# Kernel optimization log

Measured on AMD Instinct MI355X. Metric: run time of the kernel, lower is better.

Reference implementation:

```python
import jax, jax.numpy as jnp
import numpy as np

T, B, D, H = 512, 64, 512, 512

def setup_inputs() -> dict:
    key = jax.random.key(0)
    ks = jax.random.split(key, 12)
    s_in = 1.0 / np.sqrt(D + H)
    s_res = 1.0 / np.sqrt(D)
    inp = {
        'inputs': jax.random.normal(ks[0], (T, B, D), jnp.float32),
        'W_f': jax.random.uniform(ks[1], (H, D + H), jnp.float32, -s_in, s_in),
        'b_f': jax.random.uniform(ks[2], (H,), jnp.float32, -s_in, s_in),
        'W_i': jax.random.uniform(ks[3], (H, D + H), jnp.float32, -s_in, s_in),
        'b_i': jax.random.uniform(ks[4], (H,), jnp.float32, -s_in, s_in),
        'W_g': jax.random.uniform(ks[5], (H, D + H), jnp.float32, -s_in, s_in),
        'b_g': jax.random.uniform(ks[6], (H,), jnp.float32, -s_in, s_in),
        'W_o': jax.random.uniform(ks[7], (H, D + H), jnp.float32, -s_in, s_in),
        'b_o': jax.random.uniform(ks[8], (H,), jnp.float32, -s_in, s_in),
        'W_r': jax.random.uniform(ks[9], (H, D), jnp.float32, -s_res, s_res),
        'b_r': jax.random.uniform(ks[10], (H,), jnp.float32, -s_res, s_res),
    }
    return inp

def reference(inputs, W_f, b_f, W_i, b_i, W_g, b_g, W_o, b_o, W_r, b_r):
    Bsz = inputs.shape[1]
    Hd = W_f.shape[0]
    # residual projection is independent of recurrence: batch it over all timesteps
    res = jnp.einsum('tbd,hd->tbh', inputs, W_r) + b_r  # [T,B,H]

    def step(carry, xr):
        hx, cx = carry
        x, r = xr
        combined = jnp.concatenate([x, hx], axis=1)  # [B, D+H]
        f = jax.nn.sigmoid(combined @ W_f.T + b_f)
        i = jax.nn.sigmoid(combined @ W_i.T + b_i)
        g = jnp.tanh(combined @ W_g.T + b_g)
        o = jax.nn.sigmoid(combined @ W_o.T + b_o)
        cx = f * cx + i * g
        hx = o * jnp.tanh(cx) + r  # use_residual=True
        return (hx, cx), hx

    hx0 = jnp.zeros((Bsz, Hd), inputs.dtype)
    cx0 = jnp.zeros((Bsz, Hd), inputs.dtype)
    (hx, cx), stacked = jax.lax.scan(step, (hx0, cx0), (inputs, res))
    return stacked, (hx, cx)
```

## Files before the change

### kernel.cpp

```cpp
#include <hip/hip_runtime.h>


typedef __bf16         bfrag8 __attribute__((ext_vector_type(8)));
typedef float          f32x4v __attribute__((ext_vector_type(4)));
typedef unsigned short u16x8  __attribute__((ext_vector_type(8)));
typedef int            v4i    __attribute__((ext_vector_type(4)));

#define N_TB    32768
#define GXW     2560
#define OUT_HX  16777216
#define OUT_CX  16809984

__device__ __forceinline__ float bf2f(unsigned short u) {
  unsigned int x = ((unsigned int)u) << 16;
  return __builtin_bit_cast(float, x);
}
__device__ __forceinline__ unsigned short f2bf(float f) {
  unsigned int x = __builtin_bit_cast(unsigned int, f);
  x = x + 0x7FFFu + ((x >> 16) & 1u);
  return (unsigned short)(x >> 16);
}
__device__ __forceinline__ float sigf(float x) {
  x = fminf(fmaxf(x, -30.f), 30.f);
  return 1.f / (1.f + __expf(-x));
}
__device__ __forceinline__ float tanh_f(float x) {
  x = fminf(fmaxf(x, -15.f), 15.f);
  float e = __expf(-2.f * x);
  return (1.f - e) / (1.f + e);
}

__global__ void cvt_kernel(const float* __restrict__ in, unsigned short* __restrict__ out) {
  int i = (blockIdx.x * 256 + threadIdx.x) * 4;
  float4 v = *(const float4*)(in + i);
  ushort4 o = make_ushort4(f2bf(v.x), f2bf(v.y), f2bf(v.z), f2bf(v.w));
  *(ushort4*)(out + i) = o;
}

__global__ void repack_kernel(const float* __restrict__ Wf, const float* __restrict__ Wi,
                              const float* __restrict__ Wg, const float* __restrict__ Wo,
                              const float* __restrict__ Wr,
                              const float* __restrict__ bfp, const float* __restrict__ bip,
                              const float* __restrict__ bgp, const float* __restrict__ bop,
                              const float* __restrict__ brp,
                              unsigned short* __restrict__ Wc, unsigned short* __restrict__ Whx,
                              float* __restrict__ bias) {
  int tid = blockIdx.x * 256 + threadIdx.x;
  if (tid < 262144) {
    int row = tid >> 7;
    int k4  = (tid & 127) * 4;
    int g = row >> 9, h = row & 511;
    const float* W = (g == 0) ? Wf : (g == 1) ? Wi : (g == 2) ? Wg : Wo;
    float4 a = *(const float4*)(W + (size_t)h * 1024 + k4);
    float4 b = *(const float4*)(W + (size_t)h * 1024 + 512 + k4);
    *(ushort4*)(Wc  + (size_t)row * 512 + k4) = make_ushort4(f2bf(a.x), f2bf(a.y), f2bf(a.z), f2bf(a.w));
    *(ushort4*)(Whx + (size_t)row * 512 + k4) = make_ushort4(f2bf(b.x), f2bf(b.y), f2bf(b.z), f2bf(b.w));
  } else if (tid < 327680) {
    int t2 = tid - 262144;
    int row = t2 >> 7;
    int k4  = (t2 & 127) * 4;
    float4 a = *(const float4*)(Wr + (size_t)row * 512 + k4);
    *(ushort4*)(Wc + (size_t)(2048 + row) * 512 + k4) =
        make_ushort4(f2bf(a.x), f2bf(a.y), f2bf(a.z), f2bf(a.w));
  }
  if (tid < 2560) {
    float v;
    if      (tid <  512) v = bfp[tid];
    else if (tid < 1024) v = bip[tid - 512];
    else if (tid < 1536) v = bgp[tid - 1024];
    else if (tid < 2048) v = bop[tid - 1536];
    else                 v = brp[tid - 2048];
    bias[tid] = v;
  }
}

__global__ __launch_bounds__(256)
void gemm_kernel(const unsigned short* __restrict__ A, const unsigned short* __restrict__ B,
                 const float* __restrict__ bias, unsigned short* __restrict__ C) {
  const int bm = blockIdx.x;
  const int bn = blockIdx.y;
  const int tid = threadIdx.x;
  const int lane = tid & 63;
  const int w = tid >> 6;
  const int wm = w & 1, wn = w >> 1;
  const int col = lane & 15, q = lane >> 4;

  __shared__ unsigned short As[128 * 64] __attribute__((aligned(16)));
  __shared__ unsigned short Bs[128 * 64] __attribute__((aligned(16)));

  f32x4v acc[4][4] = {};

  for (int kt = 0; kt < 8; ++kt) {
    __syncthreads();
    #pragma unroll
    for (int p = 0; p < 4; ++p) {
      int idx = p * 256 + tid;
      int row = idx >> 3, gc = idx & 7;
      *(u16x8*)(&As[idx * 8]) = *(const u16x8*)(A + (size_t)(bm * 128 + row) * 512 + kt * 64 + gc * 8);
      *(u16x8*)(&Bs[idx * 8]) = *(const u16x8*)(B + (size_t)(bn * 128 + row) * 512 + kt * 64 + gc * 8);
    }
    __syncthreads();
    #pragma unroll
    for (int kk = 0; kk < 2; ++kk) {
      bfrag8 af[4], bfr[4];
      #pragma unroll
      for (int mt = 0; mt < 4; ++mt)
        af[mt] = *(const bfrag8*)(&As[(wm * 64 + mt * 16 + col) * 64 + kk * 32 + q * 8]);
      #pragma unroll
      for (int nt = 0; nt < 4; ++nt)
        bfr[nt] = *(const bfrag8*)(&Bs[(wn * 64 + nt * 16 + col) * 64 + kk * 32 + q * 8]);
      #pragma unroll
      for (int mt = 0; mt < 4; ++mt)
        #pragma unroll
        for (int nt = 0; nt < 4; ++nt)
          acc[mt][nt] = __builtin_amdgcn_mfma_f32_16x16x32_bf16(af[mt], bfr[nt], acc[mt][nt], 0, 0, 0);
    }
  }
  #pragma unroll
  for (int mt = 0; mt < 4; ++mt) {
    const int m0 = bm * 128 + wm * 64 + mt * 16 + q * 4;
    const float4 b4 = *(const float4*)(bias + m0);
    #pragma unroll
    for (int nt = 0; nt < 4; ++nt) {
      const int n = bn * 128 + wn * 64 + nt * 16 + col;
      f32x4v v = acc[mt][nt];
      ushort4 o = make_ushort4(f2bf(v[0] + b4.x), f2bf(v[1] + b4.y),
                               f2bf(v[2] + b4.z), f2bf(v[3] + b4.w));
      *(ushort4*)(C + (size_t)n * GXW + m0) = o;
    }
  }
}

__global__ __launch_bounds__(256, 1)
void recur_kernel(const unsigned short* __restrict__ Whx, const unsigned short* __restrict__ gx,
                  unsigned short* __restrict__ hbuf, int* flags, float* __restrict__ out) {
  const int jb = blockIdx.x;
  const int tid = threadIdx.x;
  const int lane = tid & 63;
  const int w = tid >> 6;
  const int gp = w & 1;
  const int mh = w >> 1;
  const int col = lane & 15;
  const int q = lane >> 4;

  __shared__ float S[2][4][64][20] __attribute__((aligned(16)));
  __shared__ unsigned short Hs[64][520] __attribute__((aligned(16)));

  bfrag8 Bf[4][8];
  #pragma unroll
  for (int g = 0; g < 4; ++g) {
    const unsigned short* wp = Whx + (size_t)(g * 512 + jb * 16 + col) * 512 + gp * 256 + q * 8;
    #pragma unroll
    for (int kk = 0; kk < 8; ++kk)
      Bf[g][kk] = *(const bfrag8*)(wp + kk * 32);
  }

  const int ub = tid >> 2;
  const int ucg = (tid & 3) * 4;
  float c4[4] = {0.f, 0.f, 0.f, 0.f};

  ushort4 gxv[4], rv;
  {
    const unsigned short* g0 = gx + (size_t)ub * GXW + jb * 16 + ucg;
    #pragma unroll
    for (int gg = 0; gg < 4; ++gg) gxv[gg] = *(const ushort4*)(g0 + gg * 512);
    rv = *(const ushort4*)(g0 + 2048);
  }

  for (int t = 0; t < 512; ++t) {
    if (t > 0) {
      if (tid < 32) {
        while (__hip_atomic_load(flags + tid, __ATOMIC_RELAXED, __HIP_MEMORY_SCOPE_AGENT) < t) {
        }
      }
      __syncthreads();
    }

    {
      const char* hsrc = (const char*)(hbuf + (t & 1) * 32768);
      v4i tmp[16];
      #pragma unroll
      for (int i = 0; i < 16; ++i) {
        const char* p = hsrc + (size_t)(i * 256 + tid) * 16;
        asm volatile("global_load_dwordx4 %0, %1, off sc0 sc1"
                     : "=v"(tmp[i]) : "v"(p) : "memory");
      }
      asm volatile("s_waitcnt vmcnt(0)" ::: "memory");
      #pragma unroll
      for (int i = 0; i < 16; ++i) {
        int idx = i * 256 + tid;
        *(v4i*)((char*)&Hs[0][0] + (size_t)(idx >> 6) * 1040 + (idx & 63) * 16) = tmp[i];
      }
    }
    __syncthreads();

    bfrag8 Af[2][8];
    #pragma unroll
    for (int mt = 0; mt < 2; ++mt) {
      const unsigned short* ap = &Hs[mh * 32 + mt * 16 + col][gp * 256 + q * 8];
      #pragma unroll
      for (int kk = 0; kk < 8; ++kk)
        Af[mt][kk] = *(const bfrag8*)(ap + kk * 32);
    }
    f32x4v acc[2][4] = {};
    #pragma unroll
    for (int kk = 0; kk < 8; ++kk)
      #pragma unroll
      for (int mt = 0; mt < 2; ++mt)
        #pragma unroll
        for (int g = 0; g < 4; ++g)
          acc[mt][g] = __builtin_amdgcn_mfma_f32_16x16x32_bf16(Af[mt][kk], Bf[g][kk], acc[mt][g], 0, 0, 0);

    #pragma unroll
    for (int mt = 0; mt < 2; ++mt)
      #pragma unroll
      for (int g = 0; g < 4; ++g) {
        const int b0 = mh * 32 + mt * 16 + q * 4;
        #pragma unroll
        for (int r = 0; r < 4; ++r)
          S[gp][g][b0 + r][col] = acc[mt][g][r];
      }
    __syncthreads();

    float pre[4][4];
    #pragma unroll
    for (int gg = 0; gg < 4; ++gg) {
      float4 s0 = *(const float4*)&S[0][gg][ub][ucg];
      float4 s1 = *(const float4*)&S[1][gg][ub][ucg];
      pre[gg][0] = s0.x + s1.x + bf2f(gxv[gg].x);
      pre[gg][1] = s0.y + s1.y + bf2f(gxv[gg].y);
      pre[gg][2] = s0.z + s1.z + bf2f(gxv[gg].z);
      pre[gg][3] = s0.w + s1.w + bf2f(gxv[gg].w);
    }
    float rres[4] = {bf2f(rv.x), bf2f(rv.y), bf2f(rv.z), bf2f(rv.w)};
    float hv[4];
    #pragma unroll
    for (int j = 0; j < 4; ++j) {
      float fg = sigf(pre[0][j]);
      float ig = sigf(pre[1][j]);
      float gg = tanh_f(pre[2][j]);
      float og = sigf(pre[3][j]);
      c4[j] = fg * c4[j] + ig * gg;
      hv[j] = og * tanh_f(c4[j]) + rres[j];
    }
    float4 h4 = make_float4(hv[0], hv[1], hv[2], hv[3]);

    if (t < 511) {
      ushort4 hb4 = make_ushort4(f2bf(hv[0]), f2bf(hv[1]), f2bf(hv[2]), f2bf(hv[3]));
      union { ushort4 u4; unsigned long long u64; } pk;
      pk.u4 = hb4;
      __hip_atomic_store((unsigned long long*)(hbuf + ((t + 1) & 1) * 32768 + ub * 512 + jb * 16 + ucg),
                         pk.u64, __ATOMIC_RELAXED, __HIP_MEMORY_SCOPE_AGENT);
      asm volatile("s_waitcnt vmcnt(0)" ::: "memory");
      __syncthreads();
      if (tid == 0)
        __hip_atomic_store(flags + jb, t + 1, __ATOMIC_RELAXED, __HIP_MEMORY_SCOPE_AGENT);
    }

    *(float4*)(out + (size_t)t * 32768 + ub * 512 + jb * 16 + ucg) = h4;

    if (t == 511) {
      *(float4*)(out + OUT_HX + ub * 512 + jb * 16 + ucg) = h4;
      *(float4*)(out + OUT_CX + ub * 512 + jb * 16 + ucg) = make_float4(c4[0], c4[1], c4[2], c4[3]);
    } else {
      const unsigned short* gn = gx + (size_t)((t + 1) * 64 + ub) * GXW + jb * 16 + ucg;
      #pragma unroll
      for (int gg = 0; gg < 4; ++gg) gxv[gg] = *(const ushort4*)(gn + gg * 512);
      rv = *(const ushort4*)(gn + 2048);
    }
  }
}

extern "C" void kernel_launch(void* const* d_in, const int* in_sizes, int n_in,
                              void* d_out, int out_size, void* d_ws, size_t ws_size,
                              hipStream_t stream) {
  const float* inputs = (const float*)d_in[0];
  const float* Wf = (const float*)d_in[1];
  const float* bf_ = (const float*)d_in[2];
  const float* Wi = (const float*)d_in[3];
  const float* bi_ = (const float*)d_in[4];
  const float* Wg = (const float*)d_in[5];
  const float* bg_ = (const float*)d_in[6];
  const float* Wo = (const float*)d_in[7];
  const float* bo_ = (const float*)d_in[8];
  const float* Wr = (const float*)d_in[9];
  const float* br_ = (const float*)d_in[10];
  float* out = (float*)d_out;

  unsigned short* X    = (unsigned short*)d_ws;
  unsigned short* Wc   = X + 16777216;
  unsigned short* Whx  = Wc + 1310720;
  float*          bias = (float*)(Whx + 1048576);
  unsigned short* gx   = (unsigned short*)(bias + 2560);
  unsigned short* hbuf = gx + 83886080;
  int*            flags = (int*)(hbuf + 65536);
  const size_t ws_needed = 206186624;
  if (ws_size < ws_needed) return;

  hipMemsetAsync(hbuf, 0, 65536 * 2 + 32 * 4, stream);

  cvt_kernel<<<16384, 256, 0, stream>>>(inputs, X);
  repack_kernel<<<1280, 256, 0, stream>>>(Wf, Wi, Wg, Wo, Wr, bf_, bi_, bg_, bo_, br_,
                                          Wc, Whx, bias);
  gemm_kernel<<<dim3(20, 256), 256, 0, stream>>>(Wc, X, bias, gx);
  recur_kernel<<<32, 256, 0, stream>>>(Whx, gx, hbuf, flags, out);
}
```

Baseline: 2.498 ms.

## Load recurrent h fragments directly from global and split gates across 8 waves

The recurrent kernel now runs 512 threads per block, with each wave owning two gates instead of four, which halves the weight fragments held per wave and the MFMAs each wave issues per step. The LDS staging of h is dropped: each wave loads its MFMA A-fragments straight from the global h buffer, which removes one LDS round trip and one block barrier per timestep. The next step's gx and residual loads are issued early, before the MFMAs, so their latency overlaps with compute. The cost is redundant global loads of h, since waves sharing rows each fetch the same data, and more threads that must meet at the remaining barriers.

```diff
diff --git a/kernel.cpp b/kernel.cpp
--- a/kernel.cpp
+++ b/kernel.cpp
@@ -131,41 +131,45 @@
   }
 }
 
-__global__ __launch_bounds__(256, 1)
+__global__ __launch_bounds__(512, 1)
 void recur_kernel(const unsigned short* __restrict__ Whx, const unsigned short* __restrict__ gx,
                   unsigned short* __restrict__ hbuf, int* flags, float* __restrict__ out) {
   const int jb = blockIdx.x;
   const int tid = threadIdx.x;
   const int lane = tid & 63;
   const int w = tid >> 6;
-  const int gp = w & 1;
-  const int mh = w >> 1;
+  const int gh = w & 1;
+  const int gp = (w >> 1) & 1;
+  const int mh = w >> 2;
   const int col = lane & 15;
   const int q = lane >> 4;
 
   __shared__ float S[2][4][64][20] __attribute__((aligned(16)));
-  __shared__ unsigned short Hs[64][520] __attribute__((aligned(16)));
-
-  bfrag8 Bf[4][8];
+
+  bfrag8 Bf[2][8];
   #pragma unroll
-  for (int g = 0; g < 4; ++g) {
-    const unsigned short* wp = Whx + (size_t)(g * 512 + jb * 16 + col) * 512 + gp * 256 + q * 8;
+  for (int g2 = 0; g2 < 2; ++g2) {
+    const int gate = gh * 2 + g2;
+    const unsigned short* wp = Whx + (size_t)(gate * 512 + jb * 16 + col) * 512 + gp * 256 + q * 8;
     #pragma unroll
     for (int kk = 0; kk < 8; ++kk)
-      Bf[g][kk] = *(const bfrag8*)(wp + kk * 32);
-  }
-
-  const int ub = tid >> 2;
-  const int ucg = (tid & 3) * 4;
-  float c4[4] = {0.f, 0.f, 0.f, 0.f};
-
-  ushort4 gxv[4], rv;
+      Bf[g2][kk] = *(const bfrag8*)(wp + kk * 32);
+  }
+
+  const int ub = tid >> 3;
+  const int uc2 = (tid & 7) * 2;
+  float c2[2] = {0.f, 0.f};
+
+  const unsigned short* gbase = gx + jb * 16 + uc2;
+  ushort2 gxv[4], rv;
   {
-    const unsigned short* g0 = gx + (size_t)ub * GXW + jb * 16 + ucg;
-    #pragma unroll
-    for (int gg = 0; gg < 4; ++gg) gxv[gg] = *(const ushort4*)(g0 + gg * 512);
-    rv = *(const ushort4*)(g0 + 2048);
-  }
+    const unsigned short* g0 = gbase + (size_t)ub * GXW;
+    #pragma unroll
+    for (int gg = 0; gg < 4; ++gg) gxv[gg] = *(const ushort2*)(g0 + gg * 512);
+    rv = *(const ushort2*)(g0 + 2048);
+  }
+
+  const int frag_off = (mh * 32 + col) * 1024 + gp * 512 + q * 16;
 
   for (int t = 0; t < 512; ++t) {
     if (t > 0) {
@@ -176,97 +180,92 @@
       __syncthreads();
     }
 
+    v4i a0[8], a1[8];
     {
-      const char* hsrc = (const char*)(hbuf + (t & 1) * 32768);
-      v4i tmp[16];
-      #pragma unroll
-      for (int i = 0; i < 16; ++i) {
-        const char* p = hsrc + (size_t)(i * 256 + tid) * 16;
-        asm volatile("global_load_dwordx4 %0, %1, off sc0 sc1"
-                     : "=v"(tmp[i]) : "v"(p) : "memory");
+      const char* hb  = (const char*)hbuf + (t & 1) * 65536 + frag_off;
+      const char* hb1 = hb + 16384;
+      #define LDA(dst, base, off) \
+        asm volatile("global_load_dwordx4 %0, %1, off offset:" #off " sc0 sc1" \
+                     : "=v"(dst) : "v"(base) : "memory");
+      LDA(a0[0], hb, 0)    LDA(a0[1], hb, 64)   LDA(a0[2], hb, 128)  LDA(a0[3], hb, 192)
+      LDA(a0[4], hb, 256)  LDA(a0[5], hb, 320)  LDA(a0[6], hb, 384)  LDA(a0[7], hb, 448)
+      LDA(a1[0], hb1, 0)   LDA(a1[1], hb1, 64)  LDA(a1[2], hb1, 128) LDA(a1[3], hb1, 192)
+      LDA(a1[4], hb1, 256) LDA(a1[5], hb1, 320) LDA(a1[6], hb1, 384) LDA(a1[7], hb1, 448)
+      #undef LDA
+      asm volatile("s_waitcnt vmcnt(0)" ::: "memory");
+    }
+
+    ushort2 ngx[4], nrv;
+    if (t < 511) {
+      const unsigned short* gn = gbase + (size_t)((t + 1) * 64 + ub) * GXW;
+      #pragma unroll
+      for (int gg = 0; gg < 4; ++gg) ngx[gg] = *(const ushort2*)(gn + gg * 512);
+      nrv = *(const ushort2*)(gn + 2048);
+    }
+
+    f32x4v acc[2][2] = {};
+    #pragma unroll
+    for (int kk = 0; kk < 8; ++kk) {
+      bfrag8 af0 = __builtin_bit_cast(bfrag8, a0[kk]);
+      bfrag8 af1 = __builtin_bit_cast(bfrag8, a1[kk]);
+      #pragma unroll
+      for (int g2 = 0; g2 < 2; ++g2) {
+        acc[0][g2] = __builtin_amdgcn_mfma_f32_16x16x32_bf16(af0, Bf[g2][kk], acc[0][g2], 0, 0, 0);
+        acc[1][g2] = __builtin_amdgcn_mfma_f32_16x16x32_bf16(af1, Bf[g2][kk], acc[1][g2], 0, 0, 0);
       }
-      asm volatile("s_waitcnt vmcnt(0)" ::: "memory");
-      #pragma unroll
-      for (int i = 0; i < 16; ++i) {
-        int idx = i * 256 + tid;
-        *(v4i*)((char*)&Hs[0][0] + (size_t)(idx >> 6) * 1040 + (idx & 63) * 16) = tmp[i];
-      }
-    }
-    __syncthreads();
-
-    bfrag8 Af[2][8];
-    #pragma unroll
-    for (int mt = 0; mt < 2; ++mt) {
-      const unsigned short* ap = &Hs[mh * 32 + mt * 16 + col][gp * 256 + q * 8];
-      #pragma unroll
-      for (int kk = 0; kk < 8; ++kk)
-        Af[mt][kk] = *(const bfrag8*)(ap + kk * 32);
-    }
-    f32x4v acc[2][4] = {};
-    #pragma unroll
-    for (int kk = 0; kk < 8; ++kk)
-      #pragma unroll
-      for (int mt = 0; mt < 2; ++mt)
-        #pragma unroll
-        for (int g = 0; g < 4; ++g)
-          acc[mt][g] = __builtin_amdgcn_mfma_f32_16x16x32_bf16(Af[mt][kk], Bf[g][kk], acc[mt][g], 0, 0, 0);
+    }
 
     #pragma unroll
     for (int mt = 0; mt < 2; ++mt)
       #pragma unroll
-      for (int g = 0; g < 4; ++g) {
+      for (int g2 = 0; g2 < 2; ++g2) {
+        const int gate = gh * 2 + g2;
         const int b0 = mh * 32 + mt * 16 + q * 4;
         #pragma unroll
         for (int r = 0; r < 4; ++r)
-          S[gp][g][b0 + r][col] = acc[mt][g][r];
+          S[gp][gate][b0 + r][col] = acc[mt][g2][r];
       }
     __syncthreads();
 
-    float pre[4][4];
+    float pre[4][2];
     #pragma unroll
     for (int gg = 0; gg < 4; ++gg) {
-      float4 s0 = *(const float4*)&S[0][gg][ub][ucg];
-      float4 s1 = *(const float4*)&S[1][gg][ub][ucg];
+      float2 s0 = *(const float2*)&S[0][gg][ub][uc2];
+      float2 s1 = *(const float2*)&S[1][gg][ub][uc2];
       pre[gg][0] = s0.x + s1.x + bf2f(gxv[gg].x);
       pre[gg][1] = s0.y + s1.y + bf2f(gxv[gg].y);
-      pre[gg][2] = s0.z + s1.z + bf2f(gxv[gg].z);
-      pre[gg][3] = s0.w + s1.w + bf2f(gxv[gg].w);
-    }
-    float rres[4] = {bf2f(rv.x), bf2f(rv.y), bf2f(rv.z), bf2f(rv.w)};
-    float hv[4];
-    #pragma unroll
-    for (int j = 0; j < 4; ++j) {
+    }
+    float rr[2] = {bf2f(rv.x), bf2f(rv.y)};
+    float hv[2];
+    #pragma unroll
+    for (int j = 0; j < 2; ++j) {
       float fg = sigf(pre[0][j]);
       float ig = sigf(pre[1][j]);
-      float gg = tanh_f(pre[2][j]);
+      float g_ = tanh_f(pre[2][j]);
       float og = sigf(pre[3][j]);
-      c4[j] = fg * c4[j] + ig * gg;
-      hv[j] = og * tanh_f(c4[j]) + rres[j];
-    }
-    float4 h4 = make_float4(hv[0], hv[1], hv[2], hv[3]);
+      c2[j] = fg * c2[j] + ig * g_;
+      hv[j] = og * tanh_f(c2[j]) + rr[j];
+    }
 
     if (t < 511) {
-      ushort4 hb4 = make_ushort4(f2bf(hv[0]), f2bf(hv[1]), f2bf(hv[2]), f2bf(hv[3]));
-      union { ushort4 u4; unsigned long long u64; } pk;
-      pk.u4 = hb4;
-      __hip_atomic_store((unsigned long long*)(hbuf + ((t + 1) & 1) * 32768 + ub * 512 + jb * 16 + ucg),
-                         pk.u64, __ATOMIC_RELAXED, __HIP_MEMORY_SCOPE_AGENT);
+      unsigned int pk = (unsigned int)f2bf(hv[0]) | ((unsigned int)f2bf(hv[1]) << 16);
+      __hip_atomic_store((unsigned int*)(hbuf + ((t + 1) & 1) * 32768 + ub * 512 + jb * 16 + uc2),
+                         pk, __ATOMIC_RELAXED, __HIP_MEMORY_SCOPE_AGENT);
       asm volatile("s_waitcnt vmcnt(0)" ::: "memory");
       __syncthreads();
       if (tid == 0)
         __hip_atomic_store(flags + jb, t + 1, __ATOMIC_RELAXED, __HIP_MEMORY_SCOPE_AGENT);
     }
 
-    *(float4*)(out + (size_t)t * 32768 + ub * 512 + jb * 16 + ucg) = h4;
+    *(float2*)(out + (size_t)t * 32768 + ub * 512 + jb * 16 + uc2) = make_float2(hv[0], hv[1]);
 
     if (t == 511) {
-      *(float4*)(out + OUT_HX + ub * 512 + jb * 16 + ucg) = h4;
-      *(float4*)(out + OUT_CX + ub * 512 + jb * 16 + ucg) = make_float4(c4[0], c4[1], c4[2], c4[3]);
+      *(float2*)(out + OUT_HX + ub * 512 + jb * 16 + uc2) = make_float2(hv[0], hv[1]);
+      *(float2*)(out + OUT_CX + ub * 512 + jb * 16 + uc2) = make_float2(c2[0], c2[1]);
     } else {
-      const unsigned short* gn = gx + (size_t)((t + 1) * 64 + ub) * GXW + jb * 16 + ucg;
-      #pragma unroll
-      for (int gg = 0; gg < 4; ++gg) gxv[gg] = *(const ushort4*)(gn + gg * 512);
-      rv = *(const ushort4*)(gn + 2048);
+      #pragma unroll
+      for (int gg = 0; gg < 4; ++gg) gxv[gg] = ngx[gg];
+      rv = nrv;
     }
   }
 }
@@ -303,5 +302,5 @@
   repack_kernel<<<1280, 256, 0, stream>>>(Wf, Wi, Wg, Wo, Wr, bf_, bi_, bg_, bo_, br_,
                                           Wc, Whx, bias);
   gemm_kernel<<<dim3(20, 256), 256, 0, stream>>>(Wc, X, bias, gx);
-  recur_kernel<<<32, 256, 0, stream>>>(Whx, gx, hbuf, flags, out);
-}
+  recur_kernel<<<32, 512, 0, stream>>>(Whx, gx, hbuf, flags, out);
+}
```

Measured after the change: 3.694 ms. 1.48x slower.
